# Optimization experiments

Hardware: AMD Instinct MI355X
Metric: run time of the kernel (lower is better)

Reference implementation:

```python
import jax, jax.numpy as jnp
import numpy as np

D = 128
N_ROUNDS = 8


def _lin(k, fan_in, fan_out):
    return jax.random.normal(k, (fan_in, fan_out), jnp.float32) * (1.0 / np.sqrt(fan_in)).astype(np.float32)


def setup_inputs() -> dict:
    key = jax.random.key(0)
    ks = jax.random.split(key, 10)
    n_vars, n_clauses, n_edges = 65536, 262144, 1048576
    n_lits = 2 * n_vars
    clause_index = jax.random.randint(ks[0], (n_edges,), 0, n_clauses)
    literal_index = jax.random.randint(ks[1], (n_edges,), 0, n_lits)
    return {
        "n_vars": n_vars,
        "n_clauses": n_clauses,
        "clause_index": clause_index,
        "literal_index": literal_index,
        "L_init_scale": jnp.float32(1.0 / np.sqrt(D)),
        "C_init_scale": jnp.float32(1.0 / np.sqrt(D)),
        "LC_scale": jnp.float32(0.1),
        "CL_scale": jnp.float32(0.1),
        # C update MLP: [C, LC_msgs] (2d) -> d -> d
        "C_W1": _lin(ks[2], 2 * D, D), "C_b1": jnp.zeros((D,), jnp.float32),
        "C_W2": _lin(ks[3], D, D),     "C_b2": jnp.zeros((D,), jnp.float32),
        # L update MLP: [L, CL_msgs, flip(L)] (3d) -> d -> d
        "L_W1": _lin(ks[4], 3 * D, D), "L_b1": jnp.zeros((D,), jnp.float32),
        "L_W2": _lin(ks[5], D, D),     "L_b2": jnp.zeros((D,), jnp.float32),
        # V score MLP: [L_pos, L_neg] (2d) -> d -> 1
        "V_W1": _lin(ks[6], 2 * D, D), "V_b1": jnp.zeros((D,), jnp.float32),
        "V_W2": _lin(ks[7], D, 1),     "V_b2": jnp.zeros((1,), jnp.float32),
    }


def _mlp(x, W1, b1, W2, b2):
    # 2-layer MLP, relu on hidden layer only
    return jnp.maximum(x @ W1 + b1, 0.0) @ W2 + b2


def reference(n_vars, n_clauses, clause_index, literal_index,
              L_init_scale, C_init_scale, LC_scale, CL_scale,
              C_W1, C_b1, C_W2, C_b2,
              L_W1, L_b1, L_W2, L_b2,
              V_W1, V_b1, V_W2, V_b2):
    d = C_W2.shape[1]
    n_lits = 2 * n_vars
    L0 = jnp.ones((n_lits, d), jnp.float32) * L_init_scale
    C0 = jnp.ones((n_clauses, d), jnp.float32) * C_init_scale

    def flip(Lm):
        # swap positive/negative literal embeddings per variable
        pl, ul = jnp.split(Lm.reshape(n_vars, 2 * d), 2, axis=1)
        return jnp.concatenate([ul, pl], axis=1).reshape(n_lits, d)

    def step(carry, _):
        L, C = carry
        # literal -> clause messages (gather + segment sum)
        LC_msgs = jax.ops.segment_sum(L[literal_index], clause_index,
                                      num_segments=n_clauses) * LC_scale
        C_new = _mlp(jnp.concatenate([C, LC_msgs], axis=-1),
                     C_W1, C_b1, C_W2, C_b2) + C  # res_layers
        # clause -> literal messages
        CL_msgs = jax.ops.segment_sum(C_new[clause_index], literal_index,
                                      num_segments=n_lits) * CL_scale
        L_new = _mlp(jnp.concatenate([L, CL_msgs, flip(L)], axis=-1),
                     L_W1, L_b1, L_W2, L_b2) + L  # res_layers
        return (L_new, C_new), None

    (L, C), _ = jax.lax.scan(step, (L0, C0), None, length=N_ROUNDS)
    V = L.reshape(n_vars, 2 * d)
    V_scores = _mlp(V, V_W1, V_b1, V_W2, V_b2)
    return V_scores[:, 0]  # pi_core_var_logits
```

## Files before the change

kernel.cpp:

```cpp
#include <hip/hip_runtime.h>
#include <cstddef>

#define D_    128
#define NV_   65536
#define NL_   131072
#define NC_   262144
#define NE_   1048576
#define NROUNDS_ 8

typedef __attribute__((ext_vector_type(4)))  short short4v;
typedef __attribute__((ext_vector_type(8)))  short short8v;
typedef __attribute__((ext_vector_type(16))) float f32x16;

__device__ __forceinline__ float4 f4_load(const float* p) { return *(const float4*)p; }
__device__ __forceinline__ void   f4_store(float* p, float4 v) { *(float4*)p = v; }
__device__ __forceinline__ float4 f4_zero() { return make_float4(0.f, 0.f, 0.f, 0.f); }
__device__ __forceinline__ float4 f4_add(float4 a, float4 b) {
    a.x += b.x; a.y += b.y; a.z += b.z; a.w += b.w; return a;
}
__device__ __forceinline__ float4 f4_scale(float4 a, float s) {
    a.x *= s; a.y *= s; a.z *= s; a.w *= s; return a;
}

__device__ __forceinline__ void micro_fma(const float4 a[4], const float4 w[4], float4 acc[4]) {
#pragma unroll
    for (int i = 0; i < 4; i++) {
        float4 av = a[i];
        acc[i].x += av.x * w[0].x; acc[i].x += av.y * w[1].x; acc[i].x += av.z * w[2].x; acc[i].x += av.w * w[3].x;
        acc[i].y += av.x * w[0].y; acc[i].y += av.y * w[1].y; acc[i].y += av.z * w[2].y; acc[i].y += av.w * w[3].y;
        acc[i].z += av.x * w[0].z; acc[i].z += av.y * w[1].z; acc[i].z += av.z * w[2].z; acc[i].z += av.w * w[3].z;
        acc[i].w += av.x * w[0].w; acc[i].w += av.y * w[1].w; acc[i].w += av.z * w[2].w; acc[i].w += av.w * w[3].w;
    }
}

template<int KD, bool FLIP>
__device__ __forceinline__ void layer1_to_H(float* Xs, float* Wcs,
        const float* __restrict__ W1, const float* __restrict__ b1, int t)
{
    const int tr = t >> 5, tc = t & 31;
    float4 acc[4];
    acc[0] = acc[1] = acc[2] = acc[3] = f4_zero();
#pragma unroll 1
    for (int kc = 0; kc < KD; kc += 32) {
        __syncthreads();
#pragma unroll
        for (int i = t; i < 1024; i += 256)
            ((float4*)Wcs)[i] = ((const float4*)W1)[kc * 32 + i];
        __syncthreads();
        const bool fl = FLIP && (kc >= 256);
        const int ab = fl ? (kc - 256) : kc;
#pragma unroll
        for (int k = 0; k < 32; k += 4) {
            float4 a[4], w[4];
#pragma unroll
            for (int i = 0; i < 4; i++) {
                int r = 4 * tr + i;
                if (fl) r ^= 1;
                a[i] = f4_load(Xs + r * 256 + ab + k);
            }
#pragma unroll
            for (int kk = 0; kk < 4; kk++)
                w[kk] = f4_load(Wcs + (k + kk) * 128 + 4 * tc);
            micro_fma(a, w, acc);
        }
    }
    float4 bv = f4_load(b1 + 4 * tc);
    __syncthreads();
#pragma unroll
    for (int i = 0; i < 4; i++) {
        float4 h;
        h.x = fmaxf(acc[i].x + bv.x, 0.f);
        h.y = fmaxf(acc[i].y + bv.y, 0.f);
        h.z = fmaxf(acc[i].z + bv.z, 0.f);
        h.w = fmaxf(acc[i].w + bv.w, 0.f);
        f4_store(Xs + (4 * tr + i) * 256 + 128 + 4 * tc, h);
    }
}

__device__ __forceinline__ unsigned short f2bf(float x) {
    unsigned u = __float_as_uint(x);
    u += 0x7fffu + ((u >> 16) & 1u);
    return (unsigned short)(u >> 16);
}
__device__ __forceinline__ float bf2f(unsigned short h) {
    return __uint_as_float(((unsigned)h) << 16);
}
__device__ __forceinline__ void split_bf(float x, unsigned short& h, unsigned short& l) {
    h = f2bf(x);
    l = f2bf(x - bf2f(h));
}
__device__ __forceinline__ void cvt4(const float4& a, short4v& h, short4v& l) {
    unsigned short h0,h1,h2,h3,l0,l1,l2,l3;
    split_bf(a.x,h0,l0); split_bf(a.y,h1,l1); split_bf(a.z,h2,l2); split_bf(a.w,h3,l3);
    h = (short4v){(short)h0,(short)h1,(short)h2,(short)h3};
    l = (short4v){(short)l0,(short)l1,(short)l2,(short)l3};
}
__device__ __forceinline__ void cvt8(const float4& a, const float4& b, short8v& h, short8v& l) {
    unsigned short h0,h1,h2,h3,h4,h5,h6,h7,l0,l1,l2,l3,l4,l5,l6,l7;
    split_bf(a.x,h0,l0); split_bf(a.y,h1,l1); split_bf(a.z,h2,l2); split_bf(a.w,h3,l3);
    split_bf(b.x,h4,l4); split_bf(b.y,h5,l5); split_bf(b.z,h6,l6); split_bf(b.w,h7,l7);
    h = (short8v){(short)h0,(short)h1,(short)h2,(short)h3,(short)h4,(short)h5,(short)h6,(short)h7};
    l = (short8v){(short)l0,(short)l1,(short)l2,(short)l3,(short)l4,(short)l5,(short)l6,(short)l7};
}

__device__ __forceinline__ int pswz(int r, int k) { return (r * 256 + k * 2) ^ ((r & 7) << 4); }

__global__ void pack_weights(const float* __restrict__ W, short* __restrict__ out, int K)
{
    int o = blockIdx.x * 256 + threadIdx.x;
    if (o >= 2 * K * 128) return;
    int i = o & 7;
    int g = o >> 3;
    int n  = g & 127;
    int kk = (g >> 7) & 3;
    int p  = (g >> 9) & 1;
    int c  = g >> 10;
    int k  = c * 32 + kk * 8 + i;
    float x = W[k * 128 + n];
    unsigned short h = f2bf(x);
    unsigned short v = p ? f2bf(x - bf2f(h)) : h;
    out[o] = (short)v;
}

__global__ void fill_kernel(float* __restrict__ L, float* __restrict__ C,
                            const float* __restrict__ lsp, const float* __restrict__ csp)
{
    const float ls = *lsp, cs = *csp;
    const size_t stride = (size_t)gridDim.x * blockDim.x;
    size_t i0 = (size_t)blockIdx.x * blockDim.x + threadIdx.x;
    const size_t nL = (size_t)NL_ * D_ / 4, nC = (size_t)NC_ * D_ / 4;
    float4 lv = make_float4(ls, ls, ls, ls), cv = make_float4(cs, cs, cs, cs);
    for (size_t i = i0; i < nL; i += stride) ((float4*)L)[i] = lv;
    for (size_t i = i0; i < nC; i += stride) ((float4*)C)[i] = cv;
}

__global__ void count_kernel(const int* __restrict__ ci, const int* __restrict__ li,
                             int* __restrict__ ccnt, int* __restrict__ lcnt)
{
    int e = blockIdx.x * 256 + threadIdx.x;
    if (e < NE_) {
        atomicAdd(&ccnt[ci[e]], 1);
        atomicAdd(&lcnt[li[e]], 1);
    }
}

__global__ void scan_block(const int* __restrict__ in, int* __restrict__ out,
                           int* __restrict__ bsum)
{
    __shared__ int sh[256];
    const int t = threadIdx.x;
    const int base = blockIdx.x * 1024 + t * 4;
    int v0 = in[base], v1 = in[base + 1], v2 = in[base + 2], v3 = in[base + 3];
    int s = v0 + v1 + v2 + v3;
    sh[t] = s;
    __syncthreads();
    for (int off = 1; off < 256; off <<= 1) {
        int y = (t >= off) ? sh[t - off] : 0;
        __syncthreads();
        sh[t] += y;
        __syncthreads();
    }
    int excl = sh[t] - s;
    out[base + 0] = excl;
    out[base + 1] = excl + v0;
    out[base + 2] = excl + v0 + v1;
    out[base + 3] = excl + v0 + v1 + v2;
    if (t == 255) bsum[blockIdx.x] = sh[255];
}

__global__ void scan_top(int* __restrict__ bs, int n)
{
    __shared__ int sh[256];
    const int t = threadIdx.x;
    int v = (t < n) ? bs[t] : 0;
    sh[t] = v;
    __syncthreads();
    for (int off = 1; off < 256; off <<= 1) {
        int y = (t >= off) ? sh[t - off] : 0;
        __syncthreads();
        sh[t] += y;
        __syncthreads();
    }
    if (t < n) bs[t] = sh[t] - v;
}

__global__ void scan_add(int* __restrict__ offs, const int* __restrict__ bs,
                         int* __restrict__ cur, int n, int total)
{
    int i = blockIdx.x * 256 + threadIdx.x;
    if (i < n) {
        int v = offs[i] + bs[i >> 10];
        offs[i] = v;
        cur[i] = v;
    }
    if (i == 0) offs[n] = total;
}

__global__ void fill_csr(const int* __restrict__ ci, const int* __restrict__ li,
                         int* __restrict__ ccur, int* __restrict__ lcur,
                         int* __restrict__ cedges, int* __restrict__ ledges)
{
    int e = blockIdx.x * 256 + threadIdx.x;
    if (e < NE_) {
        int c = ci[e], l = li[e];
        int p = atomicAdd(&ccur[c], 1); cedges[p] = l;
        int q = atomicAdd(&lcur[l], 1); ledges[q] = c;
    }
}

template<bool FLIP>
__global__ __launch_bounds__(256, 5) void update_mfma(
        float* __restrict__ Mat, const float* __restrict__ Src,
        const int* __restrict__ offs, const int* __restrict__ eidx,
        const short* __restrict__ Wp1, const float* __restrict__ b1,
        const short* __restrict__ Wp2, const float* __restrict__ b2,
        const float* __restrict__ scale_p)
{
    __shared__ __align__(16) unsigned char SM[32768];
    unsigned char* sm = SM;
    const int t = threadIdx.x;
    const int base = blockIdx.x * 32;
    const int lane = t & 63, w = t >> 6;
    const int rA = lane & 31;
    const int kg = lane >> 5;
    const int nB = w * 32 + rA;

#pragma unroll
    for (int i = t; i < 1024; i += 256) {
        int r = i >> 5, q = i & 31;
        float4 v = ((const float4*)Mat)[(size_t)base * 32 + i];
        short4v hv, lv;
        cvt4(v, hv, lv);
        *(short4v*)(sm + pswz(r, 4 * q)) = hv;
        *(short4v*)(sm + 8192 + pswz(r, 4 * q)) = lv;
    }
    short8v mh0, ml0, mh1, ml1;
    const int gr = t >> 3, gs = t & 7;
    {
        const float sc = *scale_p;
        const int row = base + gr;
        const int e0 = offs[row], e1 = offs[row + 1];
        float4 a0 = f4_zero(), a1 = f4_zero(), a2 = f4_zero(), a3 = f4_zero();
        int e = e0;
        for (; e + 1 < e1; e += 2) {
            const float* P = Src + (size_t)eidx[e] * 128 + gs * 16;
            const float* Q = Src + (size_t)eidx[e + 1] * 128 + gs * 16;
            float4 p0 = f4_load(P), p1 = f4_load(P + 4), p2 = f4_load(P + 8), p3 = f4_load(P + 12);
            float4 q0 = f4_load(Q), q1 = f4_load(Q + 4), q2 = f4_load(Q + 8), q3 = f4_load(Q + 12);
            a0 = f4_add(a0, p0); a1 = f4_add(a1, p1); a2 = f4_add(a2, p2); a3 = f4_add(a3, p3);
            a0 = f4_add(a0, q0); a1 = f4_add(a1, q1); a2 = f4_add(a2, q2); a3 = f4_add(a3, q3);
        }
        if (e < e1) {
            const float* P = Src + (size_t)eidx[e] * 128 + gs * 16;
            a0 = f4_add(a0, f4_load(P));
            a1 = f4_add(a1, f4_load(P + 4));
            a2 = f4_add(a2, f4_load(P + 8));
            a3 = f4_add(a3, f4_load(P + 12));
        }
        a0 = f4_scale(a0, sc); a1 = f4_scale(a1, sc);
        a2 = f4_scale(a2, sc); a3 = f4_scale(a3, sc);
        cvt8(a0, a1, mh0, ml0);
        cvt8(a2, a3, mh1, ml1);
    }
    __syncthreads();

    f32x16 c0, c1;
#pragma unroll
    for (int i = 0; i < 16; ++i) { c0[i] = 0.f; c1[i] = 0.f; }

#define MFMA_STEP(Wp, st, ka, ar, HB) do {                                          \
        short8v ah = *(const short8v*)(sm + (HB) + pswz((ar), (ka)));               \
        short8v al = *(const short8v*)(sm + (HB) + 8192 + pswz((ar), (ka)));        \
        const short* Wc = (Wp) + ((st) >> 1) * 8192;                                \
        const int kk = ((st) & 1) * 2 + kg;                                         \
        short8v bh = *(const short8v*)(Wc + ((size_t)(kk * 128 + nB)) * 8);         \
        short8v bl = *(const short8v*)(Wc + ((size_t)((4 + kk) * 128 + nB)) * 8);   \
        c0 = __builtin_amdgcn_mfma_f32_32x32x16_bf16(ah, bh, c0, 0, 0, 0);          \
        c1 = __builtin_amdgcn_mfma_f32_32x32x16_bf16(ah, bl, c1, 0, 0, 0);          \
        c1 = __builtin_amdgcn_mfma_f32_32x32x16_bf16(al, bh, c1, 0, 0, 0);          \
    } while (0)

#pragma unroll 2
    for (int st = 0; st < 8; ++st)
        MFMA_STEP(Wp1, st, st * 16 + kg * 8, rA, 0);
    if (FLIP) {
#pragma unroll 2
        for (int st = 16; st < 24; ++st)
            MFMA_STEP(Wp1, st, (st - 16) * 16 + kg * 8, rA ^ 1, 0);
    }
    __syncthreads();

    {
        const int k0 = 16 * gs;
        *(short8v*)(sm + pswz(gr, k0))            = mh0;
        *(short8v*)(sm + pswz(gr, k0 + 8))        = mh1;
        *(short8v*)(sm + 8192 + pswz(gr, k0))     = ml0;
        *(short8v*)(sm + 8192 + pswz(gr, k0 + 8)) = ml1;
    }
    __syncthreads();

#pragma unroll 2
    for (int st = 8; st < 16; ++st)
        MFMA_STEP(Wp1, st, (st - 8) * 16 + kg * 8, rA, 0);

    {
        const float b = b1[nB];
#pragma unroll
        for (int i = 0; i < 16; ++i) {
            int row = (i & 3) + 8 * (i >> 2) + 4 * kg;
            float h = fmaxf(c0[i] + c1[i] + b, 0.f);
            unsigned short hh, hl;
            split_bf(h, hh, hl);
            *(short*)(sm + 16384 + pswz(row, nB)) = (short)hh;
            *(short*)(sm + 24576 + pswz(row, nB)) = (short)hl;
        }
    }
    __syncthreads();

#pragma unroll
    for (int i = 0; i < 16; ++i) { c0[i] = 0.f; c1[i] = 0.f; }
#pragma unroll 2
    for (int st = 0; st < 8; ++st)
        MFMA_STEP(Wp2, st, st * 16 + kg * 8, rA, 16384);
#undef MFMA_STEP

    {
        const float b = b2[nB];
#pragma unroll
        for (int i = 0; i < 16; ++i) {
            int row = (i & 3) + 8 * (i >> 2) + 4 * kg;
            size_t gi = (size_t)(base + row) * 128 + nB;
            Mat[gi] = c0[i] + c1[i] + b + Mat[gi];
        }
    }
}

__global__ __launch_bounds__(256) void v_score(
        float* __restrict__ out, const float* __restrict__ Lmat,
        const float* __restrict__ W1, const float* __restrict__ b1,
        const float* __restrict__ W2, const float* __restrict__ b2)
{
    __shared__ float Xs[32 * 256];
    __shared__ float Wcs[32 * 128];
    const int t = threadIdx.x;
    const int base = blockIdx.x * 32;

#pragma unroll
    for (int i = t; i < 2048; i += 256)
        ((float4*)Xs)[i] = ((const float4*)Lmat)[(size_t)base * 64 + i];

    layer1_to_H<256, false>(Xs, Wcs, W1, b1, t);
    __syncthreads();
    if (t < 32) ((float4*)Wcs)[t] = ((const float4*)W2)[t];
    __syncthreads();

    const int r = t >> 3, s = t & 7;
    float sum = 0.f;
#pragma unroll
    for (int j = 0; j < 16; j++)
        sum += Xs[r * 256 + 128 + s * 16 + j] * Wcs[s * 16 + j];
    sum += __shfl_xor(sum, 1);
    sum += __shfl_xor(sum, 2);
    sum += __shfl_xor(sum, 4);
    if (s == 0) out[base + r] = sum + b2[0];
}

extern "C" void kernel_launch(void* const* d_in, const int* in_sizes, int n_in,
                              void* d_out, int out_size, void* d_ws, size_t ws_size,
                              hipStream_t stream)
{
    const int*   ci   = (const int*)d_in[2];
    const int*   li   = (const int*)d_in[3];
    const float* Lsc  = (const float*)d_in[4];
    const float* Csc  = (const float*)d_in[5];
    const float* LCsc = (const float*)d_in[6];
    const float* CLsc = (const float*)d_in[7];
    const float* C_W1 = (const float*)d_in[8];
    const float* C_b1 = (const float*)d_in[9];
    const float* C_W2 = (const float*)d_in[10];
    const float* C_b2 = (const float*)d_in[11];
    const float* L_W1 = (const float*)d_in[12];
    const float* L_b1 = (const float*)d_in[13];
    const float* L_W2 = (const float*)d_in[14];
    const float* L_b2 = (const float*)d_in[15];
    const float* V_W1 = (const float*)d_in[16];
    const float* V_b1 = (const float*)d_in[17];
    const float* V_W2 = (const float*)d_in[18];
    const float* V_b2 = (const float*)d_in[19];
    float* out = (float*)d_out;

    char* w = (char*)d_ws;
    float* Cmat  = (float*)w; w += (size_t)NC_ * D_ * 4;
    float* Lmat  = (float*)w; w += (size_t)NL_ * D_ * 4;
    int* coffs   = (int*)w;   w += (size_t)(NC_ + 1) * 4;
    int* ccur    = (int*)w;   w += (size_t)NC_ * 4;
    int* cedges  = (int*)w;   w += (size_t)NE_ * 4;
    int* loffs   = (int*)w;   w += (size_t)(NL_ + 1) * 4;
    int* lcur    = (int*)w;   w += (size_t)NL_ * 4;
    int* ledges  = (int*)w;   w += (size_t)NE_ * 4;
    int* bsumC   = (int*)w;   w += 256 * 4;
    int* bsumL   = (int*)w;   w += 256 * 4;
    short* WpC1  = (short*)w; w += (size_t)2 * 256 * 128 * 2;
    short* WpC2  = (short*)w; w += (size_t)2 * 128 * 128 * 2;
    short* WpL1  = (short*)w; w += (size_t)2 * 384 * 128 * 2;
    short* WpL2  = (short*)w; w += (size_t)2 * 128 * 128 * 2;

    hipMemsetAsync(ccur, 0, (size_t)NC_ * 4, stream);
    hipMemsetAsync(lcur, 0, (size_t)NL_ * 4, stream);

    pack_weights<<<(2 * 256 * 128) / 256, 256, 0, stream>>>(C_W1, WpC1, 256);
    pack_weights<<<(2 * 128 * 128) / 256, 256, 0, stream>>>(C_W2, WpC2, 128);
    pack_weights<<<(2 * 384 * 128) / 256, 256, 0, stream>>>(L_W1, WpL1, 384);
    pack_weights<<<(2 * 128 * 128) / 256, 256, 0, stream>>>(L_W2, WpL2, 128);

    fill_kernel<<<2048, 256, 0, stream>>>(Lmat, Cmat, Lsc, Csc);
    count_kernel<<<NE_ / 256, 256, 0, stream>>>(ci, li, ccur, lcur);

    scan_block<<<NC_ / 1024, 256, 0, stream>>>(ccur, coffs, bsumC);
    scan_top<<<1, 256, 0, stream>>>(bsumC, NC_ / 1024);
    scan_add<<<NC_ / 256, 256, 0, stream>>>(coffs, bsumC, ccur, NC_, NE_);

    scan_block<<<NL_ / 1024, 256, 0, stream>>>(lcur, loffs, bsumL);
    scan_top<<<1, 256, 0, stream>>>(bsumL, NL_ / 1024);
    scan_add<<<NL_ / 256, 256, 0, stream>>>(loffs, bsumL, lcur, NL_, NE_);

    fill_csr<<<NE_ / 256, 256, 0, stream>>>(ci, li, ccur, lcur, cedges, ledges);

    for (int r = 0; r < NROUNDS_; r++) {
        update_mfma<false><<<NC_ / 32, 256, 0, stream>>>(
            Cmat, Lmat, coffs, cedges, WpC1, C_b1, WpC2, C_b2, LCsc);
        update_mfma<true><<<NL_ / 32, 256, 0, stream>>>(
            Lmat, Cmat, loffs, ledges, WpL1, L_b1, WpL2, L_b2, CLsc);
    }
    v_score<<<NV_ / 32, 256, 0, stream>>>(out, Lmat, V_W1, V_b1, V_W2, V_b2);
}
```

Baseline: 3.026 ms.

## Overlap self-tile load with gather, merge first-layer MFMA phases, reuse residual from LDS

The kernel now loads the block's own rows of Mat into registers before the edge gather, so those loads are in flight while gathered rows are summed. The aggregated message tile is staged in a separate LDS region. This lets all 16 first-layer MFMA steps run back to back, removing one barrier and one LDS rewrite phase. The residual add now rebuilds Mat from the bf16 hi/lo pair held in LDS instead of re-reading global memory. That saves a global load but gives a residual slightly less exact than the original fp32 value.

```diff
diff --git a/kernel.cpp b/kernel.cpp
--- a/kernel.cpp
+++ b/kernel.cpp
@@ -225,22 +225,16 @@
     const int kg = lane >> 5;
     const int nB = w * 32 + rA;
 
-#pragma unroll
-    for (int i = t; i < 1024; i += 256) {
-        int r = i >> 5, q = i & 31;
-        float4 v = ((const float4*)Mat)[(size_t)base * 32 + i];
-        short4v hv, lv;
-        cvt4(v, hv, lv);
-        *(short4v*)(sm + pswz(r, 4 * q)) = hv;
-        *(short4v*)(sm + 8192 + pswz(r, 4 * q)) = lv;
-    }
-    short8v mh0, ml0, mh1, ml1;
+    float4 sv[4];
+#pragma unroll
+    for (int j = 0; j < 4; ++j)
+        sv[j] = ((const float4*)Mat)[(size_t)base * 32 + t + j * 256];
+
+    float4 a0 = f4_zero(), a1 = f4_zero(), a2 = f4_zero(), a3 = f4_zero();
     const int gr = t >> 3, gs = t & 7;
     {
-        const float sc = *scale_p;
         const int row = base + gr;
         const int e0 = offs[row], e1 = offs[row + 1];
-        float4 a0 = f4_zero(), a1 = f4_zero(), a2 = f4_zero(), a3 = f4_zero();
         int e = e0;
         for (; e + 1 < e1; e += 2) {
             const float* P = Src + (size_t)eidx[e] * 128 + gs * 16;
@@ -257,10 +251,29 @@
             a2 = f4_add(a2, f4_load(P + 8));
             a3 = f4_add(a3, f4_load(P + 12));
         }
+    }
+
+#pragma unroll
+    for (int j = 0; j < 4; ++j) {
+        int i = t + j * 256;
+        int r = i >> 5, q = i & 31;
+        short4v hv, lv;
+        cvt4(sv[j], hv, lv);
+        *(short4v*)(sm + pswz(r, 4 * q)) = hv;
+        *(short4v*)(sm + 8192 + pswz(r, 4 * q)) = lv;
+    }
+    {
+        const float sc = *scale_p;
         a0 = f4_scale(a0, sc); a1 = f4_scale(a1, sc);
         a2 = f4_scale(a2, sc); a3 = f4_scale(a3, sc);
+        short8v mh0, ml0, mh1, ml1;
         cvt8(a0, a1, mh0, ml0);
         cvt8(a2, a3, mh1, ml1);
+        const int k0 = 16 * gs;
+        *(short8v*)(sm + 16384 + pswz(gr, k0))     = mh0;
+        *(short8v*)(sm + 16384 + pswz(gr, k0 + 8)) = mh1;
+        *(short8v*)(sm + 24576 + pswz(gr, k0))     = ml0;
+        *(short8v*)(sm + 24576 + pswz(gr, k0 + 8)) = ml1;
     }
     __syncthreads();
 
@@ -268,9 +281,9 @@
 #pragma unroll
     for (int i = 0; i < 16; ++i) { c0[i] = 0.f; c1[i] = 0.f; }
 
-#define MFMA_STEP(Wp, st, ka, ar, HB) do {                                          \
-        short8v ah = *(const short8v*)(sm + (HB) + pswz((ar), (ka)));               \
-        short8v al = *(const short8v*)(sm + (HB) + 8192 + pswz((ar), (ka)));        \
+#define MFMA_STEP(Wp, st, ka, ar, AB) do {                                          \
+        short8v ah = *(const short8v*)(sm + (AB) + pswz((ar), (ka)));               \
+        short8v al = *(const short8v*)(sm + (AB) + 8192 + pswz((ar), (ka)));        \
         const short* Wc = (Wp) + ((st) >> 1) * 8192;                                \
         const int kk = ((st) & 1) * 2 + kg;                                         \
         short8v bh = *(const short8v*)(Wc + ((size_t)(kk * 128 + nB)) * 8);         \
@@ -283,25 +296,15 @@
 #pragma unroll 2
     for (int st = 0; st < 8; ++st)
         MFMA_STEP(Wp1, st, st * 16 + kg * 8, rA, 0);
+#pragma unroll 2
+    for (int st = 8; st < 16; ++st)
+        MFMA_STEP(Wp1, st, (st - 8) * 16 + kg * 8, rA, 16384);
     if (FLIP) {
 #pragma unroll 2
         for (int st = 16; st < 24; ++st)
             MFMA_STEP(Wp1, st, (st - 16) * 16 + kg * 8, rA ^ 1, 0);
     }
     __syncthreads();
-
-    {
-        const int k0 = 16 * gs;
-        *(short8v*)(sm + pswz(gr, k0))            = mh0;
-        *(short8v*)(sm + pswz(gr, k0 + 8))        = mh1;
-        *(short8v*)(sm + 8192 + pswz(gr, k0))     = ml0;
-        *(short8v*)(sm + 8192 + pswz(gr, k0 + 8)) = ml1;
-    }
-    __syncthreads();
-
-#pragma unroll 2
-    for (int st = 8; st < 16; ++st)
-        MFMA_STEP(Wp1, st, (st - 8) * 16 + kg * 8, rA, 0);
 
     {
         const float b = b1[nB];
@@ -317,6 +320,15 @@
     }
     __syncthreads();
 
+    float res[16];
+#pragma unroll
+    for (int i = 0; i < 16; ++i) {
+        int row = (i & 3) + 8 * (i >> 2) + 4 * kg;
+        unsigned short sh = *(const unsigned short*)(sm + pswz(row, nB));
+        unsigned short sl = *(const unsigned short*)(sm + 8192 + pswz(row, nB));
+        res[i] = bf2f(sh) + bf2f(sl);
+    }
+
 #pragma unroll
     for (int i = 0; i < 16; ++i) { c0[i] = 0.f; c1[i] = 0.f; }
 #pragma unroll 2
@@ -330,7 +342,7 @@
         for (int i = 0; i < 16; ++i) {
             int row = (i & 3) + 8 * (i >> 2) + 4 * kg;
             size_t gi = (size_t)(base + row) * 128 + nB;
-            Mat[gi] = c0[i] + c1[i] + b + Mat[gi];
+            Mat[gi] = c0[i] + c1[i] + b + res[i];
         }
     }
 }
```

Result: faster. 2.853 ms (-5.7%).
